# Optimization experiments

Measured on AMD Instinct MI355X. Metric: run time of the kernel, lower is better.

The kernel has to match this reference:

```python
import jax, jax.numpy as jnp
import numpy as np

V, E, H, L = 10000, 512, 1024, 2
B, S = 64, 128
STEPS = 143  # hard-coded decode loop length in the original module


def setup_inputs() -> dict:
    key = jax.random.key(0)
    ks = jax.random.split(key, 12)
    s = 0.05  # keep recurrent dynamics stable
    d = dict(
        x=jax.random.randint(ks[0], (B, S), 0, V),
        emb=jax.random.normal(ks[1], (V, E), jnp.float32) * s,
        Wih0=jax.random.normal(ks[2], (4 * H, E), jnp.float32) * s,
        Whh0=jax.random.normal(ks[3], (4 * H, H), jnp.float32) * s,
        bih0=jax.random.normal(ks[4], (4 * H,), jnp.float32) * s,
        bhh0=jax.random.normal(ks[5], (4 * H,), jnp.float32) * s,
        Wih1=jax.random.normal(ks[6], (4 * H, H), jnp.float32) * s,
        Whh1=jax.random.normal(ks[7], (4 * H, H), jnp.float32) * s,
        bih1=jax.random.normal(ks[8], (4 * H,), jnp.float32) * s,
        bhh1=jax.random.normal(ks[9], (4 * H,), jnp.float32) * s,
        Wfc=jax.random.normal(ks[10], (V, H), jnp.float32) * s,
        bfc=jax.random.normal(ks[11], (V,), jnp.float32) * s,
    )
    return d


def _cell(x, h, c, Wih, Whh, bih, bhh):
    # PyTorch LSTM gate order: i, f, g, o
    gates = x @ Wih.T + h @ Whh.T + (bih + bhh)
    i, f, g, o = jnp.split(gates, 4, axis=-1)
    c_new = jax.nn.sigmoid(f) * c + jax.nn.sigmoid(i) * jnp.tanh(g)
    h_new = jax.nn.sigmoid(o) * jnp.tanh(c_new)
    return h_new, c_new


def _stack_step(layers, inp, h, c):
    hs, cs = [], []
    for l, (Wih, Whh, bih, bhh) in enumerate(layers):
        hn, cn = _cell(inp, h[l], c[l], Wih, Whh, bih, bhh)
        hs.append(hn)
        cs.append(cn)
        inp = hn
    return jnp.stack(hs), jnp.stack(cs), inp


def reference(x, emb, Wih0, Whh0, bih0, bhh0, Wih1, Whh1, bih1, bhh1, Wfc, bfc):
    layers = [(Wih0, Whh0, bih0, bhh0), (Wih1, Whh1, bih1, bhh1)]
    b = x.shape[0]
    hd = Whh0.shape[1]
    embedded = emb[x]                      # [B, S, E]
    h0 = jnp.zeros((len(layers), b, hd), embedded.dtype)
    c0 = jnp.zeros_like(h0)

    def enc_step(carry, xt):               # xt: [B, E]
        h, c = carry
        h, c, out = _stack_step(layers, xt, h, c)
        return (h, c), out

    (h, c), outs = jax.lax.scan(enc_step, (h0, c0), jnp.swapaxes(embedded, 0, 1))
    last = outs[-1]                         # [B, H]
    first_logits = last @ Wfc.T + bfc       # [B, V]
    # Faithful quirk: argmax over the raw hidden state (dim H), used as token ids.
    tok0 = jnp.argmax(last, axis=-1)

    def dec_step(carry, _):
        h, c, tok = carry
        inp = emb[tok]                      # [B, E]
        h, c, out = _stack_step(layers, inp, h, c)
        logits = out @ Wfc.T + bfc          # [B, V]
        tok = jnp.argmax(logits, axis=-1)
        return (h, c, tok), logits

    _, dec_logits = jax.lax.scan(dec_step, (h, c, tok0), None, length=STEPS)
    # predictions: [B, 1 + STEPS, V]
    preds = jnp.concatenate([first_logits[:, None, :], jnp.swapaxes(dec_logits, 0, 1)], axis=1)
    return preds
```

## Files before the change

kernel.cpp:

```cpp
#include <hip/hip_runtime.h>
#include <cfloat>
#include <cmath>

namespace {

constexpr int Bn = 64;
constexpr int Sn = 128;
constexpr int En = 512;
constexpr int Hn = 1024;
constexpr int Vn = 10000;
constexpr int Tn = 144;
constexpr int DEC = 143;
constexpr int ENC_CHUNK = 16;

__device__ __forceinline__ double sigd(double x) { return 1.0 / (1.0 + exp(-x)); }

__global__ __launch_bounds__(256) void init_state(double* __restrict__ ws) {
    const size_t i = (size_t)blockIdx.x * blockDim.x + threadIdx.x;
    ws[i] = 0.0;
}

__global__ __launch_bounds__(256) void gather_enc(
    const int* __restrict__ x, const float* __restrict__ emb,
    float* __restrict__ xt, const int t0)
{
    const int b  = (int)blockIdx.x & 63;
    const int ti = (int)blockIdx.x >> 6;
    const int token = x[b * Sn + t0 + ti];
    const float* __restrict__ er = emb + (size_t)token * En;
    float* __restrict__ xo = xt + (size_t)ti * En * 64;
    for (int k = (int)threadIdx.x; k < En; k += 256)
        xo[(size_t)k * 64 + b] = er[k];
}

template<typename XT, int KX>
__global__ __launch_bounds__(256) void cell_kernel(
    const XT*     __restrict__ xt,
    const double* __restrict__ hin,
    double*       __restrict__ hout,
    double*       __restrict__ cst,
    const float*  __restrict__ Wih,
    const float*  __restrict__ Whh,
    const float*  __restrict__ bih,
    const float*  __restrict__ bhh)
{
    __shared__ double part[4][4][64];
    const int tid = (int)threadIdx.x;
    const int b = tid & 63;
    const int w = tid >> 6;
    const int j = (int)blockIdx.x;

    double a0 = 0.0, a1 = 0.0, a2 = 0.0, a3 = 0.0;

    {
        constexpr int C = KX / 4;
        const int k0 = w * C;
        const float4* __restrict__ r0 = (const float4*)(Wih + (size_t)(0 * Hn + j) * KX + k0);
        const float4* __restrict__ r1 = (const float4*)(Wih + (size_t)(1 * Hn + j) * KX + k0);
        const float4* __restrict__ r2 = (const float4*)(Wih + (size_t)(2 * Hn + j) * KX + k0);
        const float4* __restrict__ r3 = (const float4*)(Wih + (size_t)(3 * Hn + j) * KX + k0);
        const XT* __restrict__ xp = xt + (size_t)k0 * 64 + b;
        #pragma unroll 2
        for (int i = 0; i < C / 4; ++i) {
            const float4 w0 = r0[i], w1 = r1[i], w2 = r2[i], w3 = r3[i];
            const double x0 = (double)xp[(size_t)(4 * i + 0) * 64];
            const double x1 = (double)xp[(size_t)(4 * i + 1) * 64];
            const double x2 = (double)xp[(size_t)(4 * i + 2) * 64];
            const double x3 = (double)xp[(size_t)(4 * i + 3) * 64];
            a0 = fma(x0, (double)w0.x, a0); a0 = fma(x1, (double)w0.y, a0);
            a0 = fma(x2, (double)w0.z, a0); a0 = fma(x3, (double)w0.w, a0);
            a1 = fma(x0, (double)w1.x, a1); a1 = fma(x1, (double)w1.y, a1);
            a1 = fma(x2, (double)w1.z, a1); a1 = fma(x3, (double)w1.w, a1);
            a2 = fma(x0, (double)w2.x, a2); a2 = fma(x1, (double)w2.y, a2);
            a2 = fma(x2, (double)w2.z, a2); a2 = fma(x3, (double)w2.w, a2);
            a3 = fma(x0, (double)w3.x, a3); a3 = fma(x1, (double)w3.y, a3);
            a3 = fma(x2, (double)w3.z, a3); a3 = fma(x3, (double)w3.w, a3);
        }
    }
    {
        constexpr int C = Hn / 4;
        const int k0 = w * C;
        const float4* __restrict__ r0 = (const float4*)(Whh + (size_t)(0 * Hn + j) * Hn + k0);
        const float4* __restrict__ r1 = (const float4*)(Whh + (size_t)(1 * Hn + j) * Hn + k0);
        const float4* __restrict__ r2 = (const float4*)(Whh + (size_t)(2 * Hn + j) * Hn + k0);
        const float4* __restrict__ r3 = (const float4*)(Whh + (size_t)(3 * Hn + j) * Hn + k0);
        const double* __restrict__ hp = hin + (size_t)k0 * 64 + b;
        #pragma unroll 2
        for (int i = 0; i < C / 4; ++i) {
            const float4 w0 = r0[i], w1 = r1[i], w2 = r2[i], w3 = r3[i];
            const double x0 = hp[(size_t)(4 * i + 0) * 64];
            const double x1 = hp[(size_t)(4 * i + 1) * 64];
            const double x2 = hp[(size_t)(4 * i + 2) * 64];
            const double x3 = hp[(size_t)(4 * i + 3) * 64];
            a0 = fma(x0, (double)w0.x, a0); a0 = fma(x1, (double)w0.y, a0);
            a0 = fma(x2, (double)w0.z, a0); a0 = fma(x3, (double)w0.w, a0);
            a1 = fma(x0, (double)w1.x, a1); a1 = fma(x1, (double)w1.y, a1);
            a1 = fma(x2, (double)w1.z, a1); a1 = fma(x3, (double)w1.w, a1);
            a2 = fma(x0, (double)w2.x, a2); a2 = fma(x1, (double)w2.y, a2);
            a2 = fma(x2, (double)w2.z, a2); a2 = fma(x3, (double)w2.w, a2);
            a3 = fma(x0, (double)w3.x, a3); a3 = fma(x1, (double)w3.y, a3);
            a3 = fma(x2, (double)w3.z, a3); a3 = fma(x3, (double)w3.w, a3);
        }
    }

    part[w][0][b] = a0; part[w][1][b] = a1; part[w][2][b] = a2; part[w][3][b] = a3;
    __syncthreads();

    if (tid < 64) {
        const int bb = tid;
        const double ai = (double)bih[0 * Hn + j] + (double)bhh[0 * Hn + j]
                        + part[0][0][bb] + part[1][0][bb] + part[2][0][bb] + part[3][0][bb];
        const double af = (double)bih[1 * Hn + j] + (double)bhh[1 * Hn + j]
                        + part[0][1][bb] + part[1][1][bb] + part[2][1][bb] + part[3][1][bb];
        const double ag = (double)bih[2 * Hn + j] + (double)bhh[2 * Hn + j]
                        + part[0][2][bb] + part[1][2][bb] + part[2][2][bb] + part[3][2][bb];
        const double ao = (double)bih[3 * Hn + j] + (double)bhh[3 * Hn + j]
                        + part[0][3][bb] + part[1][3][bb] + part[2][3][bb] + part[3][3][bb];
        const double ig = sigd(ai);
        const double fg = sigd(af);
        const double gg = tanh(ag);
        const double og = sigd(ao);
        const size_t idx = (size_t)j * 64 + bb;
        const double cn = fg * cst[idx] + ig * gg;
        cst[idx] = cn;
        hout[idx] = og * tanh(cn);
    }
}

__global__ __launch_bounds__(256) void logits_kernel(
    const double* __restrict__ h,
    const float*  __restrict__ Wfc,
    const float*  __restrict__ bfc,
    float*        __restrict__ outf)
{
    __shared__ double part[4][4][64];
    const int tid = (int)threadIdx.x;
    const int b = tid & 63;
    const int w = tid >> 6;
    const int v0 = (int)blockIdx.x * 4;
    double a0 = 0.0, a1 = 0.0, a2 = 0.0, a3 = 0.0;
    const int k0 = w * (Hn / 4);
    const float4* __restrict__ r0 = (const float4*)(Wfc + (size_t)(v0 + 0) * Hn + k0);
    const float4* __restrict__ r1 = (const float4*)(Wfc + (size_t)(v0 + 1) * Hn + k0);
    const float4* __restrict__ r2 = (const float4*)(Wfc + (size_t)(v0 + 2) * Hn + k0);
    const float4* __restrict__ r3 = (const float4*)(Wfc + (size_t)(v0 + 3) * Hn + k0);
    const double* __restrict__ hp = h + (size_t)k0 * 64 + b;
    #pragma unroll 2
    for (int i = 0; i < Hn / 16; ++i) {
        const float4 w0 = r0[i], w1 = r1[i], w2 = r2[i], w3 = r3[i];
        const double x0 = hp[(size_t)(4 * i + 0) * 64];
        const double x1 = hp[(size_t)(4 * i + 1) * 64];
        const double x2 = hp[(size_t)(4 * i + 2) * 64];
        const double x3 = hp[(size_t)(4 * i + 3) * 64];
        a0 = fma(x0, (double)w0.x, a0); a0 = fma(x1, (double)w0.y, a0);
        a0 = fma(x2, (double)w0.z, a0); a0 = fma(x3, (double)w0.w, a0);
        a1 = fma(x0, (double)w1.x, a1); a1 = fma(x1, (double)w1.y, a1);
        a1 = fma(x2, (double)w1.z, a1); a1 = fma(x3, (double)w1.w, a1);
        a2 = fma(x0, (double)w2.x, a2); a2 = fma(x1, (double)w2.y, a2);
        a2 = fma(x2, (double)w2.z, a2); a2 = fma(x3, (double)w2.w, a2);
        a3 = fma(x0, (double)w3.x, a3); a3 = fma(x1, (double)w3.y, a3);
        a3 = fma(x2, (double)w3.z, a3); a3 = fma(x3, (double)w3.w, a3);
    }
    part[w][0][b] = a0; part[w][1][b] = a1; part[w][2][b] = a2; part[w][3][b] = a3;
    __syncthreads();
    const int vi = tid >> 6;
    const int bb = tid & 63;
    const double s = (double)bfc[v0 + vi]
                   + part[0][vi][bb] + part[1][vi][bb] + part[2][vi][bb] + part[3][vi][bb];
    outf[(size_t)bb * ((size_t)Tn * Vn) + v0 + vi] = (float)s;
}

template<typename T>
__global__ __launch_bounds__(256) void argmax_gather(
    const T* __restrict__ vals, const int n, const int estride, const size_t bstride,
    const float* __restrict__ emb, float* __restrict__ xt)
{
    __shared__ double sv[256];
    __shared__ int si[256];
    __shared__ int stok;
    const int tid = (int)threadIdx.x;
    const int b = (int)blockIdx.x;
    const T* __restrict__ row = vals + (size_t)b * bstride;
    double best = -DBL_MAX;
    int bi = 0x7fffffff;
    for (int k = tid; k < n; k += 256) {
        const double v = (double)row[(size_t)k * estride];
        if (v > best) { best = v; bi = k; }
    }
    sv[tid] = best; si[tid] = bi;
    __syncthreads();
    for (int s = 128; s > 0; s >>= 1) {
        if (tid < s) {
            if (sv[tid + s] > sv[tid] || (sv[tid + s] == sv[tid] && si[tid + s] < si[tid])) {
                sv[tid] = sv[tid + s];
                si[tid] = si[tid + s];
            }
        }
        __syncthreads();
    }
    if (tid == 0) stok = si[0];
    __syncthreads();
    const float* __restrict__ er = emb + (size_t)stok * En;
    for (int k = tid; k < En; k += 256)
        xt[(size_t)k * 64 + b] = er[k];
}

}

extern "C" void kernel_launch(void* const* d_in, const int* in_sizes, int n_in,
                              void* d_out, int out_size, void* d_ws, size_t ws_size,
                              hipStream_t stream)
{
    const int*   x    = (const int*)d_in[0];
    const float* emb  = (const float*)d_in[1];
    const float* Wih0 = (const float*)d_in[2];
    const float* Whh0 = (const float*)d_in[3];
    const float* bih0 = (const float*)d_in[4];
    const float* bhh0 = (const float*)d_in[5];
    const float* Wih1 = (const float*)d_in[6];
    const float* Whh1 = (const float*)d_in[7];
    const float* bih1 = (const float*)d_in[8];
    const float* bhh1 = (const float*)d_in[9];
    const float* Wfc  = (const float*)d_in[10];
    const float* bfc  = (const float*)d_in[11];
    float* out = (float*)d_out;

    double* ws = (double*)d_ws;
    const size_t BH = (size_t)Bn * Hn;
    double* h0 = ws;
    double* h1 = ws + 2 * BH;
    double* c0 = ws + 4 * BH;
    double* c1 = ws + 5 * BH;
    float*  xt = (float*)(ws + 6 * BH);

    init_state<<<1536, 256, 0, stream>>>(ws);

    int p = 0;
    for (int t0 = 0; t0 < Sn; t0 += ENC_CHUNK) {
        gather_enc<<<ENC_CHUNK * 64, 256, 0, stream>>>(x, emb, xt, t0);
        for (int ti = 0; ti < ENC_CHUNK; ++ti) {
            cell_kernel<float, En><<<Hn, 256, 0, stream>>>(
                xt + (size_t)ti * En * 64,
                h0 + (size_t)p * BH, h0 + (size_t)(1 - p) * BH, c0,
                Wih0, Whh0, bih0, bhh0);
            cell_kernel<double, Hn><<<Hn, 256, 0, stream>>>(
                h0 + (size_t)(1 - p) * BH,
                h1 + (size_t)p * BH, h1 + (size_t)(1 - p) * BH, c1,
                Wih1, Whh1, bih1, bhh1);
            p ^= 1;
        }
    }

    logits_kernel<<<2500, 256, 0, stream>>>(h1 + (size_t)p * BH, Wfc, bfc, out);
    argmax_gather<double><<<64, 256, 0, stream>>>(
        h1 + (size_t)p * BH, Hn, 64, 1, emb, xt);

    for (int s = 0; s < DEC; ++s) {
        cell_kernel<float, En><<<Hn, 256, 0, stream>>>(
            xt,
            h0 + (size_t)p * BH, h0 + (size_t)(1 - p) * BH, c0,
            Wih0, Whh0, bih0, bhh0);
        cell_kernel<double, Hn><<<Hn, 256, 0, stream>>>(
            h0 + (size_t)(1 - p) * BH,
            h1 + (size_t)p * BH, h1 + (size_t)(1 - p) * BH, c1,
            Wih1, Whh1, bih1, bhh1);
        p ^= 1;
        logits_kernel<<<2500, 256, 0, stream>>>(
            h1 + (size_t)p * BH, Wfc, bfc, out + (size_t)(1 + s) * Vn);
        if (s + 1 < DEC) {
            argmax_gather<float><<<64, 256, 0, stream>>>(
                out + (size_t)(1 + s) * Vn, Vn, 1, (size_t)Tn * Vn, emb, xt);
        }
    }

    (void)in_sizes; (void)n_in; (void)out_size; (void)ws_size;
}
```

Measured before the change: 82.59 ms.

## Retile LSTM and logits GEMVs, pre-convert weights to fp64 in workspace

Cell kernels now compute 4 hidden units per block with 512 threads, splitting K in halves, so each h/x load is reused across 16 gate rows. Logits compute 16 vocab rows per block with the full K per wave and write float4 outputs. Biases are pre-combined, and the weights are optionally converted to fp64 in the workspace (when it is large enough) to avoid per-element conversions, at the cost of doubling weight bandwidth. The xt buffers become double.

Result: slower. 131.1 ms (+58.7%).

```diff
diff --git a/kernel.cpp b/kernel.cpp
--- a/kernel.cpp
+++ b/kernel.cpp
@@ -13,6 +13,28 @@
 constexpr int DEC = 143;
 constexpr int ENC_CHUNK = 16;
 
+constexpr size_t BH = (size_t)Hn * 64;
+constexpr size_t OFF_H0A = 0;
+constexpr size_t OFF_H0B = BH;
+constexpr size_t OFF_C0  = 2 * BH;
+constexpr size_t OFF_H1A = 3 * BH;
+constexpr size_t OFF_H1B = 4 * BH;
+constexpr size_t OFF_C1  = 5 * BH;
+constexpr size_t OFF_XT  = 6 * BH;
+constexpr size_t OFF_BC0 = OFF_XT + (size_t)ENC_CHUNK * En * 64;
+constexpr size_t OFF_BC1 = OFF_BC0 + 4 * Hn;
+constexpr size_t OFF_BFC = OFF_BC1 + 4 * Hn;
+constexpr size_t OFF_W   = OFF_BFC + 10240;
+constexpr size_t N_WIH0  = (size_t)4 * Hn * En;
+constexpr size_t N_WHH   = (size_t)4 * Hn * Hn;
+constexpr size_t N_WFC   = (size_t)Vn * Hn;
+constexpr size_t OFF_WIH0 = OFF_W;
+constexpr size_t OFF_WHH0 = OFF_WIH0 + N_WIH0;
+constexpr size_t OFF_WIH1 = OFF_WHH0 + N_WHH;
+constexpr size_t OFF_WHH1 = OFF_WIH1 + N_WHH;
+constexpr size_t OFF_WFC  = OFF_WHH1 + N_WHH;
+constexpr size_t WS_NEED  = OFF_WFC + N_WFC;
+
 __device__ __forceinline__ double sigd(double x) { return 1.0 / (1.0 + exp(-x)); }
 
 __global__ __launch_bounds__(256) void init_state(double* __restrict__ ws) {
@@ -20,102 +42,116 @@
     ws[i] = 0.0;
 }
 
+__global__ __launch_bounds__(256) void cvt_f32_f64(
+    const float* __restrict__ s, double* __restrict__ d, const int n) {
+    const int stride = (int)gridDim.x * 256;
+    for (int i = (int)blockIdx.x * 256 + (int)threadIdx.x; i < n; i += stride)
+        d[i] = (double)s[i];
+}
+
+__global__ __launch_bounds__(256) void bias_combine(
+    const float* __restrict__ a, const float* __restrict__ b,
+    double* __restrict__ d, const int n) {
+    const int stride = (int)gridDim.x * 256;
+    for (int i = (int)blockIdx.x * 256 + (int)threadIdx.x; i < n; i += stride)
+        d[i] = (double)a[i] + (double)b[i];
+}
+
 __global__ __launch_bounds__(256) void gather_enc(
     const int* __restrict__ x, const float* __restrict__ emb,
-    float* __restrict__ xt, const int t0)
+    double* __restrict__ xt, const int t0)
 {
     const int b  = (int)blockIdx.x & 63;
     const int ti = (int)blockIdx.x >> 6;
     const int token = x[b * Sn + t0 + ti];
     const float* __restrict__ er = emb + (size_t)token * En;
-    float* __restrict__ xo = xt + (size_t)ti * En * 64;
+    double* __restrict__ xo = xt + (size_t)ti * En * 64;
     for (int k = (int)threadIdx.x; k < En; k += 256)
-        xo[(size_t)k * 64 + b] = er[k];
-}
-
-template<typename XT, int KX>
-__global__ __launch_bounds__(256) void cell_kernel(
-    const XT*     __restrict__ xt,
+        xo[(size_t)k * 64 + b] = (double)er[k];
+}
+
+__device__ __forceinline__ void ldw4(const double* __restrict__ p,
+                                     double& x, double& y, double& z, double& w) {
+    const double4 v = *(const double4*)p; x = v.x; y = v.y; z = v.z; w = v.w;
+}
+__device__ __forceinline__ void ldw4(const float* __restrict__ p,
+                                     double& x, double& y, double& z, double& w) {
+    const float4 v = *(const float4*)p;
+    x = (double)v.x; y = (double)v.y; z = (double)v.z; w = (double)v.w;
+}
+
+template<typename WT, int C>
+__device__ __forceinline__ void gemv4(
+    const WT* __restrict__ r0, const WT* __restrict__ r1,
+    const WT* __restrict__ r2, const WT* __restrict__ r3,
+    const double* __restrict__ xp,
+    double& a0, double& a1, double& a2, double& a3)
+{
+    #pragma unroll 2
+    for (int i = 0; i < C / 4; ++i) {
+        const size_t kk = (size_t)(4 * i) * 64;
+        const double x0 = xp[kk], x1 = xp[kk + 64], x2 = xp[kk + 128], x3 = xp[kk + 192];
+        double wx, wy, wz, ww;
+        ldw4(r0 + 4 * i, wx, wy, wz, ww);
+        a0 = fma(x0, wx, a0); a0 = fma(x1, wy, a0); a0 = fma(x2, wz, a0); a0 = fma(x3, ww, a0);
+        ldw4(r1 + 4 * i, wx, wy, wz, ww);
+        a1 = fma(x0, wx, a1); a1 = fma(x1, wy, a1); a1 = fma(x2, wz, a1); a1 = fma(x3, ww, a1);
+        ldw4(r2 + 4 * i, wx, wy, wz, ww);
+        a2 = fma(x0, wx, a2); a2 = fma(x1, wy, a2); a2 = fma(x2, wz, a2); a2 = fma(x3, ww, a2);
+        ldw4(r3 + 4 * i, wx, wy, wz, ww);
+        a3 = fma(x0, wx, a3); a3 = fma(x1, wy, a3); a3 = fma(x2, wz, a3); a3 = fma(x3, ww, a3);
+    }
+}
+
+template<typename WT, int KX>
+__global__ __launch_bounds__(512) void cell_gemm(
+    const double* __restrict__ xt,
     const double* __restrict__ hin,
     double*       __restrict__ hout,
     double*       __restrict__ cst,
-    const float*  __restrict__ Wih,
-    const float*  __restrict__ Whh,
-    const float*  __restrict__ bih,
-    const float*  __restrict__ bhh)
-{
-    __shared__ double part[4][4][64];
-    const int tid = (int)threadIdx.x;
-    const int b = tid & 63;
-    const int w = tid >> 6;
-    const int j = (int)blockIdx.x;
+    const WT*     __restrict__ Wih,
+    const WT*     __restrict__ Whh,
+    const double* __restrict__ bc)
+{
+    __shared__ double part[2][4][4][64];
+    const int tid  = (int)threadIdx.x;
+    const int b    = tid & 63;
+    const int w    = tid >> 6;
+    const int g    = w & 3;
+    const int half = w >> 2;
+    const int jt   = (int)blockIdx.x;
 
     double a0 = 0.0, a1 = 0.0, a2 = 0.0, a3 = 0.0;
 
     {
-        constexpr int C = KX / 4;
-        const int k0 = w * C;
-        const float4* __restrict__ r0 = (const float4*)(Wih + (size_t)(0 * Hn + j) * KX + k0);
-        const float4* __restrict__ r1 = (const float4*)(Wih + (size_t)(1 * Hn + j) * KX + k0);
-        const float4* __restrict__ r2 = (const float4*)(Wih + (size_t)(2 * Hn + j) * KX + k0);
-        const float4* __restrict__ r3 = (const float4*)(Wih + (size_t)(3 * Hn + j) * KX + k0);
-        const XT* __restrict__ xp = xt + (size_t)k0 * 64 + b;
-        #pragma unroll 2
-        for (int i = 0; i < C / 4; ++i) {
-            const float4 w0 = r0[i], w1 = r1[i], w2 = r2[i], w3 = r3[i];
-            const double x0 = (double)xp[(size_t)(4 * i + 0) * 64];
-            const double x1 = (double)xp[(size_t)(4 * i + 1) * 64];
-            const double x2 = (double)xp[(size_t)(4 * i + 2) * 64];
-            const double x3 = (double)xp[(size_t)(4 * i + 3) * 64];
-            a0 = fma(x0, (double)w0.x, a0); a0 = fma(x1, (double)w0.y, a0);
-            a0 = fma(x2, (double)w0.z, a0); a0 = fma(x3, (double)w0.w, a0);
-            a1 = fma(x0, (double)w1.x, a1); a1 = fma(x1, (double)w1.y, a1);
-            a1 = fma(x2, (double)w1.z, a1); a1 = fma(x3, (double)w1.w, a1);
-            a2 = fma(x0, (double)w2.x, a2); a2 = fma(x1, (double)w2.y, a2);
-            a2 = fma(x2, (double)w2.z, a2); a2 = fma(x3, (double)w2.w, a2);
-            a3 = fma(x0, (double)w3.x, a3); a3 = fma(x1, (double)w3.y, a3);
-            a3 = fma(x2, (double)w3.z, a3); a3 = fma(x3, (double)w3.w, a3);
-        }
+        constexpr int C = KX / 2;
+        const int k0 = half * C;
+        const size_t rb = ((size_t)g * Hn + (size_t)jt * 4) * KX + k0;
+        gemv4<WT, C>(Wih + rb, Wih + rb + KX, Wih + rb + 2 * KX, Wih + rb + 3 * KX,
+                     xt + (size_t)k0 * 64 + b, a0, a1, a2, a3);
     }
     {
-        constexpr int C = Hn / 4;
-        const int k0 = w * C;
-        const float4* __restrict__ r0 = (const float4*)(Whh + (size_t)(0 * Hn + j) * Hn + k0);
-        const float4* __restrict__ r1 = (const float4*)(Whh + (size_t)(1 * Hn + j) * Hn + k0);
-        const float4* __restrict__ r2 = (const float4*)(Whh + (size_t)(2 * Hn + j) * Hn + k0);
-        const float4* __restrict__ r3 = (const float4*)(Whh + (size_t)(3 * Hn + j) * Hn + k0);
-        const double* __restrict__ hp = hin + (size_t)k0 * 64 + b;
-        #pragma unroll 2
-        for (int i = 0; i < C / 4; ++i) {
-            const float4 w0 = r0[i], w1 = r1[i], w2 = r2[i], w3 = r3[i];
-            const double x0 = hp[(size_t)(4 * i + 0) * 64];
-            const double x1 = hp[(size_t)(4 * i + 1) * 64];
-            const double x2 = hp[(size_t)(4 * i + 2) * 64];
-            const double x3 = hp[(size_t)(4 * i + 3) * 64];
-            a0 = fma(x0, (double)w0.x, a0); a0 = fma(x1, (double)w0.y, a0);
-            a0 = fma(x2, (double)w0.z, a0); a0 = fma(x3, (double)w0.w, a0);
-            a1 = fma(x0, (double)w1.x, a1); a1 = fma(x1, (double)w1.y, a1);
-            a1 = fma(x2, (double)w1.z, a1); a1 = fma(x3, (double)w1.w, a1);
-            a2 = fma(x0, (double)w2.x, a2); a2 = fma(x1, (double)w2.y, a2);
-            a2 = fma(x2, (double)w2.z, a2); a2 = fma(x3, (double)w2.w, a2);
-            a3 = fma(x0, (double)w3.x, a3); a3 = fma(x1, (double)w3.y, a3);
-            a3 = fma(x2, (double)w3.z, a3); a3 = fma(x3, (double)w3.w, a3);
-        }
-    }
-
-    part[w][0][b] = a0; part[w][1][b] = a1; part[w][2][b] = a2; part[w][3][b] = a3;
+        constexpr int C = Hn / 2;
+        const int k0 = half * C;
+        const size_t rb = ((size_t)g * Hn + (size_t)jt * 4) * Hn + k0;
+        gemv4<WT, C>(Whh + rb, Whh + rb + Hn, Whh + rb + 2 * Hn, Whh + rb + 3 * Hn,
+                     hin + (size_t)k0 * 64 + b, a0, a1, a2, a3);
+    }
+
+    part[half][g][0][b] = a0;
+    part[half][g][1][b] = a1;
+    part[half][g][2][b] = a2;
+    part[half][g][3][b] = a3;
     __syncthreads();
 
-    if (tid < 64) {
-        const int bb = tid;
-        const double ai = (double)bih[0 * Hn + j] + (double)bhh[0 * Hn + j]
-                        + part[0][0][bb] + part[1][0][bb] + part[2][0][bb] + part[3][0][bb];
-        const double af = (double)bih[1 * Hn + j] + (double)bhh[1 * Hn + j]
-                        + part[0][1][bb] + part[1][1][bb] + part[2][1][bb] + part[3][1][bb];
-        const double ag = (double)bih[2 * Hn + j] + (double)bhh[2 * Hn + j]
-                        + part[0][2][bb] + part[1][2][bb] + part[2][2][bb] + part[3][2][bb];
-        const double ao = (double)bih[3 * Hn + j] + (double)bhh[3 * Hn + j]
-                        + part[0][3][bb] + part[1][3][bb] + part[2][3][bb] + part[3][3][bb];
+    if (tid < 256) {
+        const int jl = tid >> 6;
+        const int bb = tid & 63;
+        const int j  = jt * 4 + jl;
+        const double ai = bc[0 * Hn + j] + part[0][0][jl][bb] + part[1][0][jl][bb];
+        const double af = bc[1 * Hn + j] + part[0][1][jl][bb] + part[1][1][jl][bb];
+        const double ag = bc[2 * Hn + j] + part[0][2][jl][bb] + part[1][2][jl][bb];
+        const double ao = bc[3 * Hn + j] + part[0][3][jl][bb] + part[1][3][jl][bb];
         const double ig = sigd(ai);
         const double fg = sigd(af);
         const double gg = tanh(ag);
@@ -127,53 +163,44 @@
     }
 }
 
-__global__ __launch_bounds__(256) void logits_kernel(
+template<typename WT>
+__global__ __launch_bounds__(256) void logits_gemm(
     const double* __restrict__ h,
-    const float*  __restrict__ Wfc,
-    const float*  __restrict__ bfc,
+    const WT*     __restrict__ Wfc,
+    const double* __restrict__ bfcd,
     float*        __restrict__ outf)
 {
-    __shared__ double part[4][4][64];
+    __shared__ double lt[16][64];
     const int tid = (int)threadIdx.x;
     const int b = tid & 63;
     const int w = tid >> 6;
-    const int v0 = (int)blockIdx.x * 4;
+    const int v0 = (int)blockIdx.x * 16;
+
     double a0 = 0.0, a1 = 0.0, a2 = 0.0, a3 = 0.0;
-    const int k0 = w * (Hn / 4);
-    const float4* __restrict__ r0 = (const float4*)(Wfc + (size_t)(v0 + 0) * Hn + k0);
-    const float4* __restrict__ r1 = (const float4*)(Wfc + (size_t)(v0 + 1) * Hn + k0);
-    const float4* __restrict__ r2 = (const float4*)(Wfc + (size_t)(v0 + 2) * Hn + k0);
-    const float4* __restrict__ r3 = (const float4*)(Wfc + (size_t)(v0 + 3) * Hn + k0);
-    const double* __restrict__ hp = h + (size_t)k0 * 64 + b;
-    #pragma unroll 2
-    for (int i = 0; i < Hn / 16; ++i) {
-        const float4 w0 = r0[i], w1 = r1[i], w2 = r2[i], w3 = r3[i];
-        const double x0 = hp[(size_t)(4 * i + 0) * 64];
-        const double x1 = hp[(size_t)(4 * i + 1) * 64];
-        const double x2 = hp[(size_t)(4 * i + 2) * 64];
-        const double x3 = hp[(size_t)(4 * i + 3) * 64];
-        a0 = fma(x0, (double)w0.x, a0); a0 = fma(x1, (double)w0.y, a0);
-        a0 = fma(x2, (double)w0.z, a0); a0 = fma(x3, (double)w0.w, a0);
-        a1 = fma(x0, (double)w1.x, a1); a1 = fma(x1, (double)w1.y, a1);
-        a1 = fma(x2, (double)w1.z, a1); a1 = fma(x3, (double)w1.w, a1);
-        a2 = fma(x0, (double)w2.x, a2); a2 = fma(x1, (double)w2.y, a2);
-        a2 = fma(x2, (double)w2.z, a2); a2 = fma(x3, (double)w2.w, a2);
-        a3 = fma(x0, (double)w3.x, a3); a3 = fma(x1, (double)w3.y, a3);
-        a3 = fma(x2, (double)w3.z, a3); a3 = fma(x3, (double)w3.w, a3);
-    }
-    part[w][0][b] = a0; part[w][1][b] = a1; part[w][2][b] = a2; part[w][3][b] = a3;
+    const size_t rb = ((size_t)v0 + (size_t)w * 4) * Hn;
+    gemv4<WT, Hn>(Wfc + rb, Wfc + rb + Hn, Wfc + rb + 2 * Hn, Wfc + rb + 3 * Hn,
+                  h + b, a0, a1, a2, a3);
+
+    lt[w * 4 + 0][b] = a0 + bfcd[v0 + w * 4 + 0];
+    lt[w * 4 + 1][b] = a1 + bfcd[v0 + w * 4 + 1];
+    lt[w * 4 + 2][b] = a2 + bfcd[v0 + w * 4 + 2];
+    lt[w * 4 + 3][b] = a3 + bfcd[v0 + w * 4 + 3];
     __syncthreads();
-    const int vi = tid >> 6;
-    const int bb = tid & 63;
-    const double s = (double)bfc[v0 + vi]
-                   + part[0][vi][bb] + part[1][vi][bb] + part[2][vi][bb] + part[3][vi][bb];
-    outf[(size_t)bb * ((size_t)Tn * Vn) + v0 + vi] = (float)s;
+
+    const int bb = tid >> 2;
+    const int vl = (tid & 3) * 4;
+    float4 o;
+    o.x = (float)lt[vl + 0][bb];
+    o.y = (float)lt[vl + 1][bb];
+    o.z = (float)lt[vl + 2][bb];
+    o.w = (float)lt[vl + 3][bb];
+    *(float4*)(outf + (size_t)bb * ((size_t)Tn * Vn) + v0 + vl) = o;
 }
 
 template<typename T>
 __global__ __launch_bounds__(256) void argmax_gather(
     const T* __restrict__ vals, const int n, const int estride, const size_t bstride,
-    const float* __restrict__ emb, float* __restrict__ xt)
+    const float* __restrict__ emb, double* __restrict__ xt)
 {
     __shared__ double sv[256];
     __shared__ int si[256];
@@ -202,7 +229,52 @@
     __syncthreads();
     const float* __restrict__ er = emb + (size_t)stok * En;
     for (int k = tid; k < En; k += 256)
-        xt[(size_t)k * 64 + b] = er[k];
+        xt[(size_t)k * 64 + b] = (double)er[k];
+}
+
+template<typename WT>
+void run_pipeline(const int* x, const float* emb,
+                  const WT* Wih0, const WT* Whh0, const WT* Wih1, const WT* Whh1,
+                  const WT* Wfc,
+                  double* ws, float* out, hipStream_t stream)
+{
+    double* h0s[2] = { ws + OFF_H0A, ws + OFF_H0B };
+    double* h1s[2] = { ws + OFF_H1A, ws + OFF_H1B };
+    double* c0 = ws + OFF_C0;
+    double* c1 = ws + OFF_C1;
+    double* xt = ws + OFF_XT;
+    const double* bc0  = ws + OFF_BC0;
+    const double* bc1  = ws + OFF_BC1;
+    const double* bfcd = ws + OFF_BFC;
+
+    int p = 0;
+    for (int t0 = 0; t0 < Sn; t0 += ENC_CHUNK) {
+        gather_enc<<<ENC_CHUNK * 64, 256, 0, stream>>>(x, emb, xt, t0);
+        for (int ti = 0; ti < ENC_CHUNK; ++ti) {
+            cell_gemm<WT, En><<<Hn / 4, 512, 0, stream>>>(
+                xt + (size_t)ti * En * 64, h0s[p], h0s[1 - p], c0, Wih0, Whh0, bc0);
+            cell_gemm<WT, Hn><<<Hn / 4, 512, 0, stream>>>(
+                h0s[1 - p], h1s[p], h1s[1 - p], c1, Wih1, Whh1, bc1);
+            p ^= 1;
+        }
+    }
+
+    logits_gemm<WT><<<Vn / 16, 256, 0, stream>>>(h1s[p], Wfc, bfcd, out);
+    argmax_gather<double><<<64, 256, 0, stream>>>(h1s[p], Hn, 64, 1, emb, xt);
+
+    for (int s = 0; s < DEC; ++s) {
+        cell_gemm<WT, En><<<Hn / 4, 512, 0, stream>>>(
+            xt, h0s[p], h0s[1 - p], c0, Wih0, Whh0, bc0);
+        cell_gemm<WT, Hn><<<Hn / 4, 512, 0, stream>>>(
+            h0s[1 - p], h1s[p], h1s[1 - p], c1, Wih1, Whh1, bc1);
+        p ^= 1;
+        logits_gemm<WT><<<Vn / 16, 256, 0, stream>>>(
+            h1s[p], Wfc, bfcd, out + (size_t)(1 + s) * Vn);
+        if (s + 1 < DEC) {
+            argmax_gather<float><<<64, 256, 0, stream>>>(
+                out + (size_t)(1 + s) * Vn, Vn, 1, (size_t)Tn * Vn, emb, xt);
+        }
+    }
 }
 
 }
@@ -224,54 +296,27 @@
     const float* Wfc  = (const float*)d_in[10];
     const float* bfc  = (const float*)d_in[11];
     float* out = (float*)d_out;
-
     double* ws = (double*)d_ws;
-    const size_t BH = (size_t)Bn * Hn;
-    double* h0 = ws;
-    double* h1 = ws + 2 * BH;
-    double* c0 = ws + 4 * BH;
-    double* c1 = ws + 5 * BH;
-    float*  xt = (float*)(ws + 6 * BH);
 
     init_state<<<1536, 256, 0, stream>>>(ws);
 
-    int p = 0;
-    for (int t0 = 0; t0 < Sn; t0 += ENC_CHUNK) {
-        gather_enc<<<ENC_CHUNK * 64, 256, 0, stream>>>(x, emb, xt, t0);
-        for (int ti = 0; ti < ENC_CHUNK; ++ti) {
-            cell_kernel<float, En><<<Hn, 256, 0, stream>>>(
-                xt + (size_t)ti * En * 64,
-                h0 + (size_t)p * BH, h0 + (size_t)(1 - p) * BH, c0,
-                Wih0, Whh0, bih0, bhh0);
-            cell_kernel<double, Hn><<<Hn, 256, 0, stream>>>(
-                h0 + (size_t)(1 - p) * BH,
-                h1 + (size_t)p * BH, h1 + (size_t)(1 - p) * BH, c1,
-                Wih1, Whh1, bih1, bhh1);
-            p ^= 1;
-        }
-    }
-
-    logits_kernel<<<2500, 256, 0, stream>>>(h1 + (size_t)p * BH, Wfc, bfc, out);
-    argmax_gather<double><<<64, 256, 0, stream>>>(
-        h1 + (size_t)p * BH, Hn, 64, 1, emb, xt);
-
-    for (int s = 0; s < DEC; ++s) {
-        cell_kernel<float, En><<<Hn, 256, 0, stream>>>(
-            xt,
-            h0 + (size_t)p * BH, h0 + (size_t)(1 - p) * BH, c0,
-            Wih0, Whh0, bih0, bhh0);
-        cell_kernel<double, Hn><<<Hn, 256, 0, stream>>>(
-            h0 + (size_t)(1 - p) * BH,
-            h1 + (size_t)p * BH, h1 + (size_t)(1 - p) * BH, c1,
-            Wih1, Whh1, bih1, bhh1);
-        p ^= 1;
-        logits_kernel<<<2500, 256, 0, stream>>>(
-            h1 + (size_t)p * BH, Wfc, bfc, out + (size_t)(1 + s) * Vn);
-        if (s + 1 < DEC) {
-            argmax_gather<float><<<64, 256, 0, stream>>>(
-                out + (size_t)(1 + s) * Vn, Vn, 1, (size_t)Tn * Vn, emb, xt);
-        }
-    }
-
-    (void)in_sizes; (void)n_in; (void)out_size; (void)ws_size;
-}
+    bias_combine<<<16, 256, 0, stream>>>(bih0, bhh0, ws + OFF_BC0, 4 * Hn);
+    bias_combine<<<16, 256, 0, stream>>>(bih1, bhh1, ws + OFF_BC1, 4 * Hn);
+    cvt_f32_f64<<<40, 256, 0, stream>>>(bfc, ws + OFF_BFC, Vn);
+
+    const bool wf64 = ws_size >= WS_NEED * sizeof(double);
+    if (wf64) {
+        cvt_f32_f64<<<4096, 256, 0, stream>>>(Wih0, ws + OFF_WIH0, (int)N_WIH0);
+        cvt_f32_f64<<<4096, 256, 0, stream>>>(Whh0, ws + OFF_WHH0, (int)N_WHH);
+        cvt_f32_f64<<<4096, 256, 0, stream>>>(Wih1, ws + OFF_WIH1, (int)N_WHH);
+        cvt_f32_f64<<<4096, 256, 0, stream>>>(Whh1, ws + OFF_WHH1, (int)N_WHH);
+        cvt_f32_f64<<<4096, 256, 0, stream>>>(Wfc,  ws + OFF_WFC,  (int)N_WFC);
+        run_pipeline<double>(x, emb,
+                             ws + OFF_WIH0, ws + OFF_WHH0, ws + OFF_WIH1, ws + OFF_WHH1,
+                             ws + OFF_WFC, ws, out, stream);
+    } else {
+        run_pipeline<float>(x, emb, Wih0, Whh0, Wih1, Whh1, Wfc, ws, out, stream);
+    }
+
+    (void)in_sizes; (void)n_in; (void)out_size;
+}
```
